# Kernel tuning notes

Hardware: AMD Instinct MI355X
Metric: run time of the kernel (lower is better)

The kernel has to match this reference:

```python
import jax, jax.numpy as jnp
import numpy as np

# Model dims (match init_kwargs)
D, L = 64, 262144          # data_size
G, J = 8, 8                # number of relations, dims per relation
FG = 16                    # filters (kernel_size) per relation
W = 31                     # window_size
PAD1 = (W - 1) // 2        # 15, left padding in the original code
F = G * FG                 # 128 total filters


def setup_inputs() -> dict:
    key = jax.random.key(0)
    k1, k2 = jax.random.split(key)
    x = jax.random.normal(k1, (D, L), dtype=jnp.float32)
    # original uses torch.rand for Parameter init -> uniform [0,1)
    params = jax.random.uniform(k2, (G, FG, J, W), dtype=jnp.float32)
    # dim_relation = [[0..7],[8..15],...,[56..63]] == arange reshaped
    rel_idx = jnp.arange(G * J, dtype=jnp.int32).reshape(G, J)
    return {"x": x, "params": params, "rel_idx": rel_idx}


def _forward(x, params, rel_idx):
    xg = x[rel_idx]                                   # [G, J, L] gather relation dims

    # Interior positions (PAD1 <= k <= L-W+PAD1): full-window correlation.
    # Expressed as a grouped 1D conv (lax conv is cross-correlation, matching
    # the original data*kernel elementwise-sum, no kernel flip).
    lhs = xg.reshape(1, G * J, L)                     # [N=1, C=G*J, L]
    rhs = params.reshape(G * FG, J, W)                # [O=G*FG, I=J, W]
    y = jax.lax.conv_general_dilated(
        lhs, rhs, window_strides=(1,),
        padding=[(PAD1, W - 1 - PAD1)],
        dimension_numbers=("NCH", "OIH", "NCH"),
        feature_group_count=G,
    )[0].reshape(G, FG, L)

    # Left boundary (k < PAD1): the original aligns kernel[0] with x[...,0]
    # and truncates BOTH at k+W-PAD1, i.e. y[k] = sum_{w < k+W-PAD1} xg[:, :, w]*K[..., w]
    # (NOT zero padding). Cumulative sum over w gives all prefixes at once.
    pl = jnp.einsum("gjw,gfjw->gfw", xg[:, :, :W], params)      # [G, FG, W]
    left_c = jnp.cumsum(pl, axis=-1)
    y = y.at[:, :, :PAD1].set(left_c[:, :, W - PAD1 - 1: W - 1])

    # Right boundary (k > L-W+PAD1): kernel[-1] aligned with x[..., L-1],
    # truncated at the front: y[k] = sum_{w >= W-m} xg[:, :, L-W+w]*K[..., w],
    # with m = L-k+PAD1. Reverse cumsum gives all suffixes.
    pr = jnp.einsum("gjw,gfjw->gfw", xg[:, :, L - W:], params)  # [G, FG, W]
    right_c = jnp.cumsum(pr[:, :, ::-1], axis=-1)[:, :, ::-1]    # suffix sums
    n_right = W - 1 - PAD1                                       # positions k = L-W+PAD1+1 .. L-1
    y = y.at[:, :, L - n_right:].set(right_c[:, :, 1: W - PAD1])

    return y.reshape(F * L, 1)                        # matches y.view(-1, 1)


def reference(x, params, rel_idx):
    return _forward(x, params, rel_idx)
```

## Files before the change

kernel.cpp:

```cpp
#include <hip/hip_runtime.h>

#define LL    262144
#define GG    8
#define JJ    8
#define FGF   16
#define WW    31
#define PAD1  15
#define CHUNK 256
#define CPW   2
#define WAVES 4
#define NTHR  (WAVES * 64)
#define SPAN  (WAVES * CPW * CHUNK)
#define NBX   (LL / SPAN)
#define SLOTS 288

typedef __bf16 bf16x8 __attribute__((ext_vector_type(8)));
typedef float  f32x4  __attribute__((ext_vector_type(4)));

__device__ inline unsigned short f2bf(float f) {
    unsigned int u = __float_as_uint(f);
    u = (u + 0x7FFF + ((u >> 16) & 1)) >> 16;
    return (unsigned short)u;
}

__global__ __launch_bounds__(NTHR, 4)
void conv_mfma(const float* __restrict__ x, const float* __restrict__ p,
               const int* __restrict__ rel, float* __restrict__ out)
{
    __shared__ unsigned short pw[32 * 16 * 8];
    __shared__ unsigned short xs[WAVES][SLOTS * 8];

    const int t = threadIdx.x;
    const int g = blockIdx.y;

    const long r0 = rel[g * JJ + 0], r1 = rel[g * JJ + 1];
    const long r2 = rel[g * JJ + 2], r3 = rel[g * JJ + 3];
    const long r4 = rel[g * JJ + 4], r5 = rel[g * JJ + 5];
    const long r6 = rel[g * JJ + 6], r7 = rel[g * JJ + 7];

    {
        const float* pg = p + (long)g * FGF * JJ * WW;
        #pragma unroll
        for (int k = 0; k < 16; ++k) {
            int i = t + k * NTHR;
            int w = i >> 7;
            int f = (i >> 3) & 15;
            int j = i & 7;
            float v = (w < WW) ? pg[(f * JJ + j) * WW + w] : 0.0f;
            pw[i] = f2bf(v);
        }
    }
    __syncthreads();

    const int lane = t & 63;
    const int wid  = t >> 6;
    const int col  = lane & 15;
    const int q    = lane >> 4;

    bf16x8 b[8];
    #pragma unroll
    for (int s = 0; s < 8; ++s)
        b[s] = *(const bf16x8*)&pw[((s * 4 + q) * 16 + col) * 8];

    unsigned short* xsl = &xs[wid][0];
    const int pb = col + q + 1;
    #define LDS8(pos) (*(const bf16x8*)&xsl[(pos) * 8])

    #pragma unroll
    for (int c = 0; c < CPW; ++c) {
        const long W0 = (long)blockIdx.x * SPAN + (wid * CPW + c) * CHUNK;

        #pragma unroll
        for (int pn = 0; pn < 5; ++pn) {
            int pp = pn * 64 + lane;
            if (pp < SLOTS) {
                long gp = W0 - 16 + pp;
                uint4 pk;
                if (gp >= 0 && gp < LL) {
                    float v0 = x[r0 * LL + gp], v1 = x[r1 * LL + gp];
                    float v2 = x[r2 * LL + gp], v3 = x[r3 * LL + gp];
                    float v4 = x[r4 * LL + gp], v5 = x[r5 * LL + gp];
                    float v6 = x[r6 * LL + gp], v7 = x[r7 * LL + gp];
                    pk.x = (unsigned)f2bf(v0) | ((unsigned)f2bf(v1) << 16);
                    pk.y = (unsigned)f2bf(v2) | ((unsigned)f2bf(v3) << 16);
                    pk.z = (unsigned)f2bf(v4) | ((unsigned)f2bf(v5) << 16);
                    pk.w = (unsigned)f2bf(v6) | ((unsigned)f2bf(v7) << 16);
                } else {
                    pk.x = pk.y = pk.z = pk.w = 0u;
                }
                *(uint4*)&xsl[pp * 8] = pk;
            }
        }

        bf16x8 F0a = LDS8(pb + 0), F0b = LDS8(pb + 4),
               F0c = LDS8(pb + 8), F0d = LDS8(pb + 12);
        #pragma unroll
        for (int T = 0; T < 16; ++T) {
            const int o = pb + T * 16 + 16;
            bf16x8 F1a = LDS8(o + 0), F1b = LDS8(o + 4),
                   F1c = LDS8(o + 8), F1d = LDS8(o + 12);

            f32x4 acc = {0.f, 0.f, 0.f, 0.f};
            acc = __builtin_amdgcn_mfma_f32_16x16x32_bf16(F0a, b[0], acc, 0, 0, 0);
            acc = __builtin_amdgcn_mfma_f32_16x16x32_bf16(F0b, b[1], acc, 0, 0, 0);
            acc = __builtin_amdgcn_mfma_f32_16x16x32_bf16(F0c, b[2], acc, 0, 0, 0);
            acc = __builtin_amdgcn_mfma_f32_16x16x32_bf16(F0d, b[3], acc, 0, 0, 0);
            acc = __builtin_amdgcn_mfma_f32_16x16x32_bf16(F1a, b[4], acc, 0, 0, 0);
            acc = __builtin_amdgcn_mfma_f32_16x16x32_bf16(F1b, b[5], acc, 0, 0, 0);
            acc = __builtin_amdgcn_mfma_f32_16x16x32_bf16(F1c, b[6], acc, 0, 0, 0);
            acc = __builtin_amdgcn_mfma_f32_16x16x32_bf16(F1d, b[7], acc, 0, 0, 0);

            const long kc0 = W0 + (long)T * 16 + q * 4;
            const size_t ro = (size_t)(g * FGF + col) * LL;
            *(f32x4*)&out[ro + kc0] = acc;

            F0a = F1a; F0b = F1b; F0c = F1c; F0d = F1d;
        }
    }
    #undef LDS8

    if (blockIdx.x == 0 || blockIdx.x == NBX - 1) {
        __syncthreads();
        const int f  = t >> 4;
        const int qq = t & 15;
        if (qq < PAD1) {
            const bool left = (blockIdx.x == 0);
            float a = 0.0f;
            for (int j = 0; j < JJ; ++j) {
                const float* pf = p + (((long)(g * FGF + f)) * JJ + j) * WW;
                const float* xj = x + (long)rel[g * JJ + j] * LL + (left ? 0 : LL - WW);
                #pragma unroll
                for (int w = 0; w < WW; ++w) {
                    bool use = left ? (w <= qq + PAD1) : (w >= qq + 1);
                    if (use) a += xj[w] * pf[w];
                }
            }
            const size_t ro = (size_t)(g * FGF + f) * LL;
            out[ro + (left ? (long)qq : (long)(LL - PAD1) + qq)] = a;
        }
    }
}

extern "C" void kernel_launch(void* const* d_in, const int* in_sizes, int n_in,
                              void* d_out, int out_size, void* d_ws, size_t ws_size,
                              hipStream_t stream)
{
    const float* x   = (const float*)d_in[0];
    const float* p   = (const float*)d_in[1];
    const int*   rel = (const int*)d_in[2];
    float* out = (float*)d_out;

    dim3 grid(NBX, GG);
    conv_mfma<<<grid, NTHR, 0, stream>>>(x, p, rel, out);
}
```

Baseline: 232.2 us.

## Stage MFMA outputs in LDS for coalesced stores and batch input loads

MFMA results are now written into a per-wave LDS tile, and after every 8 tiles each filter row of 128 outputs is written out as contiguous float2 stores. Before, each lane wrote scattered 16-byte pieces across 16 output rows. The global x loads for all 5 slot groups are also issued up front with clamped addresses, so they can be in flight together before conversion. This costs more LDS (about 8 KB per wave, which can lower occupancy) and more registers for the staged values. Same-wave LDS reuse happens without explicit barriers.

```diff
diff --git a/kernel.cpp b/kernel.cpp
--- a/kernel.cpp
+++ b/kernel.cpp
@@ -13,6 +13,7 @@
 #define SPAN  (WAVES * CPW * CHUNK)
 #define NBX   (LL / SPAN)
 #define SLOTS 288
+#define PADX  130
 
 typedef __bf16 bf16x8 __attribute__((ext_vector_type(8)));
 typedef float  f32x4  __attribute__((ext_vector_type(4)));
@@ -29,6 +30,7 @@
 {
     __shared__ unsigned short pw[32 * 16 * 8];
     __shared__ unsigned short xs[WAVES][SLOTS * 8];
+    __shared__ float xo[WAVES][16 * PADX];
 
     const int t = threadIdx.x;
     const int g = blockIdx.y;
@@ -63,6 +65,7 @@
         b[s] = *(const bf16x8*)&pw[((s * 4 + q) * 16 + col) * 8];
 
     unsigned short* xsl = &xs[wid][0];
+    float*          xol = &xo[wid][0];
     const int pb = col + q + 1;
     #define LDS8(pos) (*(const bf16x8*)&xsl[(pos) * 8])
 
@@ -70,24 +73,28 @@
     for (int c = 0; c < CPW; ++c) {
         const long W0 = (long)blockIdx.x * SPAN + (wid * CPW + c) * CHUNK;
 
+        float v[5][8];
         #pragma unroll
         for (int pn = 0; pn < 5; ++pn) {
-            int pp = pn * 64 + lane;
+            int  pp = pn * 64 + lane;
+            long gp = W0 - 16 + pp;
+            long gc = (gp >= 0 && gp < LL && pp < SLOTS) ? gp : 0;
+            v[pn][0] = x[r0 * LL + gc]; v[pn][1] = x[r1 * LL + gc];
+            v[pn][2] = x[r2 * LL + gc]; v[pn][3] = x[r3 * LL + gc];
+            v[pn][4] = x[r4 * LL + gc]; v[pn][5] = x[r5 * LL + gc];
+            v[pn][6] = x[r6 * LL + gc]; v[pn][7] = x[r7 * LL + gc];
+        }
+        #pragma unroll
+        for (int pn = 0; pn < 5; ++pn) {
+            int  pp = pn * 64 + lane;
+            long gp = W0 - 16 + pp;
+            bool ok = (gp >= 0 && gp < LL);
             if (pp < SLOTS) {
-                long gp = W0 - 16 + pp;
                 uint4 pk;
-                if (gp >= 0 && gp < LL) {
-                    float v0 = x[r0 * LL + gp], v1 = x[r1 * LL + gp];
-                    float v2 = x[r2 * LL + gp], v3 = x[r3 * LL + gp];
-                    float v4 = x[r4 * LL + gp], v5 = x[r5 * LL + gp];
-                    float v6 = x[r6 * LL + gp], v7 = x[r7 * LL + gp];
-                    pk.x = (unsigned)f2bf(v0) | ((unsigned)f2bf(v1) << 16);
-                    pk.y = (unsigned)f2bf(v2) | ((unsigned)f2bf(v3) << 16);
-                    pk.z = (unsigned)f2bf(v4) | ((unsigned)f2bf(v5) << 16);
-                    pk.w = (unsigned)f2bf(v6) | ((unsigned)f2bf(v7) << 16);
-                } else {
-                    pk.x = pk.y = pk.z = pk.w = 0u;
-                }
+                pk.x = ok ? ((unsigned)f2bf(v[pn][0]) | ((unsigned)f2bf(v[pn][1]) << 16)) : 0u;
+                pk.y = ok ? ((unsigned)f2bf(v[pn][2]) | ((unsigned)f2bf(v[pn][3]) << 16)) : 0u;
+                pk.z = ok ? ((unsigned)f2bf(v[pn][4]) | ((unsigned)f2bf(v[pn][5]) << 16)) : 0u;
+                pk.w = ok ? ((unsigned)f2bf(v[pn][6]) | ((unsigned)f2bf(v[pn][7]) << 16)) : 0u;
                 *(uint4*)&xsl[pp * 8] = pk;
             }
         }
@@ -110,9 +117,16 @@
             acc = __builtin_amdgcn_mfma_f32_16x16x32_bf16(F1c, b[6], acc, 0, 0, 0);
             acc = __builtin_amdgcn_mfma_f32_16x16x32_bf16(F1d, b[7], acc, 0, 0, 0);
 
-            const long kc0 = W0 + (long)T * 16 + q * 4;
-            const size_t ro = (size_t)(g * FGF + col) * LL;
-            *(f32x4*)&out[ro + kc0] = acc;
+            *(f32x4*)&xol[col * PADX + (T & 7) * 16 + q * 4] = acc;
+
+            if ((T & 7) == 7) {
+                const long fp0 = W0 + (long)(T >> 3) * 128;
+                #pragma unroll
+                for (int f = 0; f < 16; ++f) {
+                    float2 vv = *(const float2*)&xol[f * PADX + lane * 2];
+                    *(float2*)&out[(size_t)(g * FGF + f) * LL + fp0 + lane * 2] = vv;
+                }
+            }
 
             F0a = F1a; F0b = F1b; F0c = F1c; F0d = F1d;
         }
```

New measurement: 214.5 us. -7.6%, faster.
